# Kernel optimization log

Measured on AMD Instinct MI355X. Metric: run time of the kernel, lower is better.

Reference implementation:

```python
import jax, jax.numpy as jnp
import numpy as np

D_MODEL = 512
D_STATE = 64
BATCH = 8
SEQ_L = 4096


def setup_inputs() -> dict:
    key = jax.random.key(0)
    k_u, k_c, k_d = jax.random.split(key, 3)
    u = jax.random.normal(k_u, (BATCH, D_MODEL, SEQ_L), dtype=jnp.float32)
    # B buffer: zeros with first state column = 1 (fixed shift-SSM input matrix)
    B = jnp.zeros((D_MODEL, D_STATE), dtype=jnp.float32).at[:, 0].set(1.0)
    C = jax.random.normal(k_c, (1, D_MODEL, D_STATE), dtype=jnp.float32)
    D = jax.random.normal(k_d, (D_MODEL,), dtype=jnp.float32)
    return {"u": u, "B": B, "C": C, "D": D}


def reference(u, B, C, D):
    """Shift state-space layer. u: (batch, H, L) -> (batch, H, L)."""
    L = u.shape[-1]
    n = 2 * L  # pad to 2L so circular conv == linear (causal) conv
    B_fc = jnp.conj(jnp.fft.rfft(B, n=n))            # (H, n//2+1)
    C_f = jnp.fft.rfft(C, n=n)                       # (1, H, n//2+1)
    kernel = jnp.fft.irfft(B_fc * C_f, n=n)[..., :L]  # (1, H, L)
    kernel_f = jnp.fft.rfft(kernel, n=n)             # (1, H, n//2+1)
    u_f = jnp.fft.rfft(u, n=n)                       # (batch, H, n//2+1)
    y = jnp.fft.irfft(u_f * kernel_f, n=n)[..., :L]  # (batch, H, L)
    return y + u * D[:, None]
```

## Files before the change

### kernel.cpp

```cpp
#include <hip/hip_runtime.h>
#include <hip/hip_bf16.h>


#define D_MODEL 512
#define D_STATE 64
#define BATCH   8
#define SEQ_L   4096
#define NT      256

__device__ __forceinline__ int SW(int g) { return g ^ ((g >> 3) & 7); }

__global__ void __launch_bounds__(NT)
shift_fused_kernel(const float* __restrict__ u,
                   const float* __restrict__ B,
                   const float* __restrict__ C,
                   const float* __restrict__ D,
                   float* __restrict__ y) {
    const int row = blockIdx.x;
    const int h   = row & (D_MODEL - 1);
    const float* __restrict__ urow = u + (size_t)row * SEQ_L;
    float* __restrict__ yrow       = y + (size_t)row * SEQ_L;

    __shared__ float  K[D_STATE];
    __shared__ float4 su4[(D_STATE + SEQ_L) / 4];

    const int t = threadIdx.x;

    if (t < 16) su4[SW(t)] = make_float4(0.f, 0.f, 0.f, 0.f);

    #pragma unroll
    for (int j = 0; j < 4; ++j) {
        const int e = t + NT * j;
        const float4 v = *(const float4*)(urow + 4 * e);
        su4[SW(16 + e)] = v;
    }

    if (t < D_STATE) {
        const float* Bh = B + h * D_STATE;
        const float* Ch = C + h * D_STATE;
        float s = 0.f;
        #pragma unroll
        for (int j = 0; j < D_STATE; ++j) {
            const int c = t + j;
            float bv = Bh[j];
            const float cv = Ch[c & (D_STATE - 1)];
            if (c >= D_STATE) bv = 0.f;
            s = fmaf(bv, cv, s);
        }
        if (t == 0) s += D[h];
        K[t] = s;
    }
    __syncthreads();

    const int out0 = t * 16;
    const float* sf = (const float*)su4;

    float acc[16];
    #pragma unroll
    for (int i = 0; i < 16; ++i) acc[i] = 0.f;

    #pragma unroll
    for (int kk = 0; kk < 4; ++kk) {
        const int base = out0 + 48 - 16 * kk;
        const int g0   = base >> 2;
        float win[32];
        #pragma unroll
        for (int w = 0; w < 8; ++w) {
            const float4 v = *(const float4*)(sf + 4 * SW(g0 + w));
            win[4*w + 0] = v.x; win[4*w + 1] = v.y;
            win[4*w + 2] = v.z; win[4*w + 3] = v.w;
        }
        #pragma unroll
        for (int q = 0; q < 16; ++q) {
            const float Kv = K[16 * kk + q];
            #pragma unroll
            for (int i = 0; i < 16; ++i)
                acc[i] = fmaf(Kv, win[16 + i - q], acc[i]);
        }
    }

    #pragma unroll
    for (int j = 0; j < 4; ++j) {
        float4 o;
        o.x = acc[4*j + 0]; o.y = acc[4*j + 1];
        o.z = acc[4*j + 2]; o.w = acc[4*j + 3];
        *(float4*)(yrow + out0 + 4*j) = o;
    }
}

extern "C" void kernel_launch(void* const* d_in, const int* in_sizes, int n_in,
                              void* d_out, int out_size, void* d_ws, size_t ws_size,
                              hipStream_t stream) {
    const float* u = (const float*)d_in[0];
    const float* B = (const float*)d_in[1];
    const float* C = (const float*)d_in[2];
    const float* D = (const float*)d_in[3];
    float* y = (float*)d_out;

    shift_fused_kernel<<<dim3(BATCH * D_MODEL), dim3(NT), 0, stream>>>(u, B, C, D, y);
}
```

Before: 138.9 us.

## Load convolution windows directly from global into registers, drop LDS staging

Removes the shared-memory staging of the whole input row. Each thread now loads its overlapping 16-element windows straight from global memory (through L1/L2) into rotating register buffers, interleaved with the FMA chunks. The B and C vectors are staged in LDS with a zero-padded C so the kernel-tap computation needs no branch, and launch bounds now request 4 blocks per SM. The trade-off is redundant global reads, since each element is fetched by up to five threads, plus higher register pressure, in exchange for no LDS traffic and more occupancy.

Measured after the change: 157.4 us. 1.13x slower.

```diff
diff --git a/kernel.cpp b/kernel.cpp
--- a/kernel.cpp
+++ b/kernel.cpp
@@ -8,76 +8,89 @@
 #define SEQ_L   4096
 #define NT      256
 
-__device__ __forceinline__ int SW(int g) { return g ^ ((g >> 3) & 7); }
-
-__global__ void __launch_bounds__(NT)
-shift_fused_kernel(const float* __restrict__ u,
-                   const float* __restrict__ B,
-                   const float* __restrict__ C,
-                   const float* __restrict__ D,
-                   float* __restrict__ y) {
+__global__ void __launch_bounds__(NT, 4)
+shift_fused(const float* __restrict__ u,
+            const float* __restrict__ B,
+            const float* __restrict__ C,
+            const float* __restrict__ D,
+            float* __restrict__ y) {
     const int row = blockIdx.x;
     const int h   = row & (D_MODEL - 1);
     const float* __restrict__ urow = u + (size_t)row * SEQ_L;
     float* __restrict__ yrow       = y + (size_t)row * SEQ_L;
 
-    __shared__ float  K[D_STATE];
-    __shared__ float4 su4[(D_STATE + SEQ_L) / 4];
+    __shared__ float Bs[D_STATE];
+    __shared__ float Cs[2 * D_STATE];
+    __shared__ float K[D_STATE];
 
-    const int t = threadIdx.x;
+    const int t    = threadIdx.x;
+    const int out0 = t << 4;
 
-    if (t < 16) su4[SW(t)] = make_float4(0.f, 0.f, 0.f, 0.f);
+    float wa[16], wb[16], wc[16];
+    auto load16 = [&](float* w, int base) {
+        if (base >= 0) {
+            #pragma unroll
+            for (int j = 0; j < 4; ++j) {
+                const float4 v = *(const float4*)(urow + base + 4 * j);
+                w[4*j + 0] = v.x; w[4*j + 1] = v.y;
+                w[4*j + 2] = v.z; w[4*j + 3] = v.w;
+            }
+        } else {
+            #pragma unroll
+            for (int j = 0; j < 16; ++j) w[j] = 0.f;
+        }
+    };
+    load16(wa, out0);
+    load16(wb, out0 - 16);
+    load16(wc, out0 - 32);
 
-    #pragma unroll
-    for (int j = 0; j < 4; ++j) {
-        const int e = t + NT * j;
-        const float4 v = *(const float4*)(urow + 4 * e);
-        su4[SW(16 + e)] = v;
+    if (t < 16) {
+        ((float4*)Bs)[t] = ((const float4*)(B + h * D_STATE))[t];
+    } else if (t < 48) {
+        const int j = t - 16;
+        ((float4*)Cs)[j] = (j < 16) ? ((const float4*)(C + h * D_STATE))[j]
+                                    : make_float4(0.f, 0.f, 0.f, 0.f);
     }
-
+    __syncthreads();
     if (t < D_STATE) {
-        const float* Bh = B + h * D_STATE;
-        const float* Ch = C + h * D_STATE;
         float s = 0.f;
         #pragma unroll
-        for (int j = 0; j < D_STATE; ++j) {
-            const int c = t + j;
-            float bv = Bh[j];
-            const float cv = Ch[c & (D_STATE - 1)];
-            if (c >= D_STATE) bv = 0.f;
-            s = fmaf(bv, cv, s);
-        }
+        for (int j = 0; j < D_STATE; ++j)
+            s = fmaf(Bs[j], Cs[t + j], s);
         if (t == 0) s += D[h];
         K[t] = s;
     }
     __syncthreads();
 
-    const int out0 = t * 16;
-    const float* sf = (const float*)su4;
-
     float acc[16];
     #pragma unroll
     for (int i = 0; i < 16; ++i) acc[i] = 0.f;
 
-    #pragma unroll
-    for (int kk = 0; kk < 4; ++kk) {
-        const int base = out0 + 48 - 16 * kk;
-        const int g0   = base >> 2;
-        float win[32];
+    const float4* K4 = (const float4*)K;
+    auto chunk = [&](int kk, const float* hi, const float* lo) {
         #pragma unroll
-        for (int w = 0; w < 8; ++w) {
-            const float4 v = *(const float4*)(sf + 4 * SW(g0 + w));
-            win[4*w + 0] = v.x; win[4*w + 1] = v.y;
-            win[4*w + 2] = v.z; win[4*w + 3] = v.w;
+        for (int qj = 0; qj < 4; ++qj) {
+            const float4 kv = K4[4 * kk + qj];
+            const float kq[4] = {kv.x, kv.y, kv.z, kv.w};
+            #pragma unroll
+            for (int qq = 0; qq < 4; ++qq) {
+                const int q = 4 * qj + qq;
+                #pragma unroll
+                for (int i = 0; i < 16; ++i) {
+                    const int widx = 16 + i - q;
+                    const float wv = (widx >= 16) ? hi[widx - 16] : lo[widx];
+                    acc[i] = fmaf(kq[qq], wv, acc[i]);
+                }
+            }
         }
-        #pragma unroll
-        for (int q = 0; q < 16; ++q) {
-            const float Kv = K[16 * kk + q];
-            #pragma unroll
-            for (int i = 0; i < 16; ++i)
-                acc[i] = fmaf(Kv, win[16 + i - q], acc[i]);
-        }
-    }
+    };
+
+    chunk(0, wa, wb);
+    load16(wa, out0 - 48);
+    chunk(1, wb, wc);
+    load16(wb, out0 - 64);
+    chunk(2, wc, wa);
+    chunk(3, wa, wb);
 
     #pragma unroll
     for (int j = 0; j < 4; ++j) {
@@ -97,5 +110,5 @@
     const float* D = (const float*)d_in[3];
     float* y = (float*)d_out;
 
-    shift_fused_kernel<<<dim3(BATCH * D_MODEL), dim3(NT), 0, stream>>>(u, B, C, D, y);
+    shift_fused<<<dim3(BATCH * D_MODEL), dim3(NT), 0, stream>>>(u, B, C, D, y);
 }
```

## Compute shift-SSM convolution with bf16 MFMA Toeplitz matmul

Applied to the files above, without the earlier changes.

Replaces the per-thread fp32 FMA sliding-window convolution with MFMA 16x16x32 bf16 instructions. The input row is converted to bf16 in swizzled LDS, and the 64-tap kernel is laid out as a Toeplitz B-fragment held in registers. The kernel taps are now built from B and C staged in shared memory. The aim is to move the 64-tap dot products onto the matrix cores and cut the scalar FMA and LDS-read work. In exchange, rounding inputs and kernel to bf16 lowers accuracy, and the output stores become narrow scattered writes instead of float4.

Measured after the change: 120.4 us. -13.4%, faster.

```diff
diff --git a/kernel.cpp b/kernel.cpp
--- a/kernel.cpp
+++ b/kernel.cpp
@@ -8,83 +8,100 @@
 #define SEQ_L   4096
 #define NT      256
 
+typedef short           s16x8 __attribute__((ext_vector_type(8)));
+typedef unsigned short  u16;
+typedef u16             u16x4 __attribute__((ext_vector_type(4)));
+typedef u16             u16x8 __attribute__((ext_vector_type(8)));
+typedef float           f32x4 __attribute__((ext_vector_type(4)));
+
 __device__ __forceinline__ int SW(int g) { return g ^ ((g >> 3) & 7); }
 
+__device__ __forceinline__ u16 f2bf(float f) {
+    unsigned v = __builtin_bit_cast(unsigned, f);
+    return (u16)((v + 0x7FFFu + ((v >> 16) & 1u)) >> 16);
+}
+
 __global__ void __launch_bounds__(NT)
-shift_fused_kernel(const float* __restrict__ u,
-                   const float* __restrict__ B,
-                   const float* __restrict__ C,
-                   const float* __restrict__ D,
-                   float* __restrict__ y) {
+shift_mfma(const float* __restrict__ u, const float* __restrict__ B,
+           const float* __restrict__ C, const float* __restrict__ D,
+           float* __restrict__ y) {
     const int row = blockIdx.x;
     const int h   = row & (D_MODEL - 1);
     const float* __restrict__ urow = u + (size_t)row * SEQ_L;
     float* __restrict__ yrow       = y + (size_t)row * SEQ_L;
 
-    __shared__ float  K[D_STATE];
-    __shared__ float4 su4[(D_STATE + SEQ_L) / 4];
+    __shared__ u16   ub[536 * 8];
+    __shared__ float Bs[64];
+    __shared__ float Cs[128];
+    __shared__ float Kf[64];
 
     const int t = threadIdx.x;
 
-    if (t < 16) su4[SW(t)] = make_float4(0.f, 0.f, 0.f, 0.f);
-
-    #pragma unroll
-    for (int j = 0; j < 4; ++j) {
-        const int e = t + NT * j;
-        const float4 v = *(const float4*)(urow + 4 * e);
-        su4[SW(16 + e)] = v;
-    }
-
-    if (t < D_STATE) {
-        const float* Bh = B + h * D_STATE;
-        const float* Ch = C + h * D_STATE;
-        float s = 0.f;
-        #pragma unroll
-        for (int j = 0; j < D_STATE; ++j) {
-            const int c = t + j;
-            float bv = Bh[j];
-            const float cv = Ch[c & (D_STATE - 1)];
-            if (c >= D_STATE) bv = 0.f;
-            s = fmaf(bv, cv, s);
-        }
-        if (t == 0) s += D[h];
-        K[t] = s;
-    }
-    __syncthreads();
-
-    const int out0 = t * 16;
-    const float* sf = (const float*)su4;
-
-    float acc[16];
-    #pragma unroll
-    for (int i = 0; i < 16; ++i) acc[i] = 0.f;
-
-    #pragma unroll
-    for (int kk = 0; kk < 4; ++kk) {
-        const int base = out0 + 48 - 16 * kk;
-        const int g0   = base >> 2;
-        float win[32];
-        #pragma unroll
-        for (int w = 0; w < 8; ++w) {
-            const float4 v = *(const float4*)(sf + 4 * SW(g0 + w));
-            win[4*w + 0] = v.x; win[4*w + 1] = v.y;
-            win[4*w + 2] = v.z; win[4*w + 3] = v.w;
-        }
-        #pragma unroll
-        for (int q = 0; q < 16; ++q) {
-            const float Kv = K[16 * kk + q];
-            #pragma unroll
-            for (int i = 0; i < 16; ++i)
-                acc[i] = fmaf(Kv, win[16 + i - q], acc[i]);
-        }
+    if (t < 16) {
+        ((float4*)Bs)[t] = ((const float4*)(B + h * D_STATE))[t];
+    } else if (t < 48) {
+        const int j = t - 16;
+        ((float4*)Cs)[j] = (j < 16) ? ((const float4*)(C + h * D_STATE))[j]
+                                    : make_float4(0.f, 0.f, 0.f, 0.f);
     }
 
     #pragma unroll
     for (int j = 0; j < 4; ++j) {
-        float4 o;
-        o.x = acc[4*j + 0]; o.y = acc[4*j + 1];
-        o.z = acc[4*j + 2]; o.w = acc[4*j + 3];
-        *(float4*)(yrow + out0 + 4*j) = o;
+        const float4 v = *(const float4*)(urow + 4 * t + 1024 * j);
+        u16x4 pk = { f2bf(v.x), f2bf(v.y), f2bf(v.z), f2bf(v.w) };
+        const int byte = 128 + 8 * t + 2048 * j;
+        const int sb   = (SW(byte >> 4) << 4) | (byte & 8);
+        *(u16x4*)((char*)ub + sb) = pk;
+    }
+    if (t < 8) {
+        u16x8 z = {0,0,0,0,0,0,0,0};
+        *(u16x8*)((char*)ub + (SW(t) << 4)) = z;
+    } else if (t < 20) {
+        u16x8 z = {0,0,0,0,0,0,0,0};
+        const int g = 520 + (t - 8);
+        *(u16x8*)((char*)ub + (SW(g) << 4)) = z;
+    }
+    __syncthreads();
+
+    if (t < D_STATE) {
+        float s = 0.f;
+        #pragma unroll
+        for (int j = 0; j < D_STATE; ++j) s = fmaf(Bs[j], Cs[t + j], s);
+        if (t == 0) s += D[h];
+        Kf[t] = s;
+    }
+    __syncthreads();
+
+    const int l = t & 63;
+    const int n = l & 15;
+    const int q = l >> 4;
+    s16x8 bfr[3];
+    #pragma unroll
+    for (int c = 0; c < 3; ++c) {
+        #pragma unroll
+        for (int j = 0; j < 8; ++j) {
+            const int p = 32 * c + 8 * q + j;
+            const int k = 64 + n - p;
+            const float v = (k >= 0 && k < D_STATE) ? Kf[k] : 0.f;
+            bfr[c][j] = (short)f2bf(v);
+        }
+    }
+
+    const int wbase = 1024 * (t >> 6);
+    #pragma unroll
+    for (int tt = 0; tt < 4; ++tt) {
+        const int base = wbase + 256 * tt;
+        f32x4 acc = {0.f, 0.f, 0.f, 0.f};
+        #pragma unroll
+        for (int c = 0; c < 3; ++c) {
+            const int L  = base + 16 * n + 32 * c + 8 * q;
+            const int sb = SW(L >> 3) << 4;
+            const s16x8 a = *(const s16x8*)((const char*)ub + sb);
+            acc = __builtin_amdgcn_mfma_f32_16x16x32_bf16(a, bfr[c], acc, 0, 0, 0);
+        }
+        #pragma unroll
+        for (int r = 0; r < 4; ++r)
+            yrow[base + 16 * (4 * q + r) + n] = acc[r];
     }
 }
 
@@ -97,5 +114,5 @@
     const float* D = (const float*)d_in[3];
     float* y = (float*)d_out;
 
-    shift_fused_kernel<<<dim3(BATCH * D_MODEL), dim3(NT), 0, stream>>>(u, B, C, D, y);
+    shift_mfma<<<dim3(BATCH * D_MODEL), dim3(NT), 0, stream>>>(u, B, C, D, y);
 }
```
